# Kernel optimization log

Hardware: AMD Instinct MI355X
Metric: run time of the kernel (lower is better)

The kernel has to match this reference:

```python
import jax, jax.numpy as jnp
import numpy as np

B, N, D, H, P = 8, 1025, 768, 12, 32  # n = P*P + 1 (CLS + patches)
HD = D // H
EPS = 1e-5


def setup_inputs() -> dict:
    key = jax.random.key(0)
    ks = jax.random.split(key, 6)
    return {
        "x": jax.random.normal(ks[0], (B, N, D), dtype=jnp.float32),
        "canny": jax.random.uniform(ks[1], (B, 1, P, P), dtype=jnp.float32),
        "noise": jax.random.uniform(ks[2], (B, P, P), dtype=jnp.float32),
        "ln_w": jnp.ones((D,), dtype=jnp.float32),
        "ln_b": jnp.zeros((D,), dtype=jnp.float32),
        "w_qkv": (jax.random.normal(ks[3], (D, 3 * D), dtype=jnp.float32) * 0.02),
        "w_out": (jax.random.normal(ks[4], (D, D), dtype=jnp.float32) * 0.02),
        "b_out": jnp.zeros((D,), dtype=jnp.float32),
    }


def reference(x, canny, noise, ln_w, ln_b, w_qkv, w_out, b_out):
    b, n, d = x.shape
    # LayerNorm
    mu = jnp.mean(x, axis=-1, keepdims=True)
    var = jnp.mean(jnp.square(x - mu), axis=-1, keepdims=True)
    x_norm = (x - mu) * jax.lax.rsqrt(var + EPS) * ln_w + ln_b
    # QKV projection (no bias), split into heads: [b, n, 3, h, hd]
    qkv = (x_norm @ w_qkv).reshape(b, n, 3, H, HD)
    q = jnp.transpose(qkv[:, :, 0], (0, 2, 1, 3))  # [b, h, n, hd]
    k = jnp.transpose(qkv[:, :, 1], (0, 2, 1, 3))
    v = jnp.transpose(qkv[:, :, 2], (0, 2, 1, 3))
    # NOTE: source uses scale = dim ** -0.5 (full dim, not head_dim)
    dots = jnp.einsum('bhid,bhjd->bhij', q, k) * (d ** -0.5)
    # CLS-row prior injection: softmax over patch keys of CLS query row
    attn_row = jax.nn.softmax(dots[:, :, 0, 1:], axis=-1)  # [b, h, n-1]
    canny_flat = canny.reshape(b, -1) + 1.0                # [b, n-1]
    canny_flat = canny_flat / jnp.sum(canny_flat, axis=-1, keepdims=True)
    noise_flat = noise.reshape(b, -1)                      # [b, n-1]
    noise_flat = noise_flat / jnp.sum(noise_flat, axis=-1, keepdims=True)
    attn_row = attn_row + canny_flat[:, None, :] + noise_flat[:, None, :]
    dots = dots.at[:, :, 0, 1:].set(attn_row)
    # Second (full) softmax; dropout is identity in eval mode
    attn = jax.nn.softmax(dots, axis=-1)
    out = jnp.einsum('bhij,bhjd->bhid', attn, v)           # [b, h, n, hd]
    out = jnp.transpose(out, (0, 2, 1, 3)).reshape(b, n, d)
    return out @ w_out + b_out
```

## Files before the change

### kernel.cpp

```cpp
#include <hip/hip_runtime.h>

#define B_ 8
#define N_ 1025
#define D_ 768
#define H_ 12
#define NP_ 1024
#define ROWS_ (B_*N_)
#define ROWS_PAD_ 8320
#define QKVC_ 2304
#define SCALE_ 0.03608439182435161f
#define EPS_ 1e-5f

typedef float f32x4 __attribute__((ext_vector_type(4)));
typedef short s16x8 __attribute__((ext_vector_type(8)));

#define GLD16(g, l) __builtin_amdgcn_global_load_lds( \
    (const __attribute__((address_space(1))) unsigned int*)(g), \
    (__attribute__((address_space(3))) unsigned int*)(l), 16, 0, 0)

__device__ __forceinline__ float blo(unsigned int u){
  union { unsigned int i; float f; } v; v.i = u << 16; return v.f;
}
__device__ __forceinline__ float bhi(unsigned int u){
  union { unsigned int i; float f; } v; v.i = u & 0xffff0000u; return v.f;
}
__device__ __forceinline__ float bf2f(unsigned short u){
  union { unsigned int i; float f; } v; v.i = ((unsigned int)u) << 16; return v.f;
}
__device__ __forceinline__ unsigned short f2bf(float f){
  union { unsigned int i; float f; } v; v.f = f;
  unsigned int b = v.i;
  b = b + 0x7fffu + ((b >> 16) & 1u);
  return (unsigned short)(b >> 16);
}
__device__ __forceinline__ unsigned int pkbf2(float a, float b){
  union { float f; unsigned int i; } ua, ub;
  ua.f = a; ub.f = b;
  return __builtin_amdgcn_perm(ub.i + 0x8000u, ua.i + 0x8000u, 0x07060302u);
}

__global__ __launch_bounds__(256) void transpose_f2b2(
    const float* __restrict__ w1, unsigned short* __restrict__ d1,
    const float* __restrict__ w2, unsigned short* __restrict__ d2) {
  __shared__ unsigned short tile[32][33];
  int bx = blockIdx.x;
  const float* src; unsigned short* dst; int N, nb;
  if (bx < 72) { src = w1; dst = d1; N = QKVC_; nb = bx * 32; }
  else         { src = w2; dst = d2; N = D_;    nb = (bx - 72) * 32; }
  int kb = blockIdx.y * 32;
  int tx = threadIdx.x & 31, ty = threadIdx.x >> 5;
  #pragma unroll
  for (int i = 0; i < 4; i++) {
    int r = ty + i * 8;
    tile[r][tx] = f2bf(src[(size_t)(kb + r) * N + nb + tx]);
  }
  __syncthreads();
  #pragma unroll
  for (int i = 0; i < 4; i++) {
    int r = ty + i * 8;
    dst[(size_t)(nb + r) * D_ + kb + tx] = tile[tx][r];
  }
}

__global__ __launch_bounds__(256) void layernorm_k(
    const float* __restrict__ x, const float* __restrict__ w,
    const float* __restrict__ b, unsigned short* __restrict__ xn) {
  int row = blockIdx.x;
  int t = threadIdx.x;
  const float* xr = x + (size_t)row * D_;
  float v0 = xr[t], v1 = xr[t + 256], v2 = xr[t + 512];
  float s = v0 + v1 + v2;
  float q = v0 * v0 + v1 * v1 + v2 * v2;
  #pragma unroll
  for (int off = 32; off > 0; off >>= 1) {
    s += __shfl_xor(s, off, 64);
    q += __shfl_xor(q, off, 64);
  }
  __shared__ float r8[8];
  int wv = t >> 6;
  if ((t & 63) == 0) { r8[wv] = s; r8[4 + wv] = q; }
  __syncthreads();
  s = r8[0] + r8[1] + r8[2] + r8[3];
  q = r8[4] + r8[5] + r8[6] + r8[7];
  float mean = s * (1.0f / 768.0f);
  float var = q * (1.0f / 768.0f) - mean * mean;
  var = var < 0.f ? 0.f : var;
  float rstd = rsqrtf(var + EPS_);
  unsigned short* yr = xn + (size_t)row * D_;
  yr[t]       = f2bf((v0 - mean) * rstd * w[t]       + b[t]);
  yr[t + 256] = f2bf((v1 - mean) * rstd * w[t + 256] + b[t + 256]);
  yr[t + 512] = f2bf((v2 - mean) * rstd * w[t + 512] + b[t + 512]);
}

template <bool OF32>
__global__ __launch_bounds__(256) void gemm_bt(
    const unsigned short* __restrict__ A, const unsigned short* __restrict__ Bt,
    void* __restrict__ Cv, const float* __restrict__ bias,
    int Mvalid, int Nn, int Kk) {
  __shared__ short sh[16384];
  short (*As)[4096] = (short (*)[4096])sh;
  short (*Bs)[4096] = (short (*)[4096])(sh + 8192);
  int t = threadIdx.x;
  int bm = blockIdx.y * 128, bn = blockIdx.x * 128;
  int lane = t & 63, wave = t >> 6;
  int wm = (wave & 1) * 64, wn = (wave >> 1) * 64;
  int m16 = lane & 15, quad = lane >> 4;
  f32x4 acc[4][4];
  #pragma unroll
  for (int i = 0; i < 4; i++)
    #pragma unroll
    for (int j = 0; j < 4; j++) acc[i][j] = (f32x4){0.f, 0.f, 0.f, 0.f};

  int e0 = t * 8;
  int e1 = (t + 256) * 8;
  int r0 = e0 >> 5, c0 = e0 & 31;
  int r1 = e1 >> 5, c1 = e1 & 31;
  const unsigned short* a0p = A + (size_t)(bm + r0) * Kk + c0;
  const unsigned short* a1p = A + (size_t)(bm + r1) * Kk + c1;
  const unsigned short* b0p = Bt + (size_t)(bn + r0) * Kk + c0;
  const unsigned short* b1p = Bt + (size_t)(bn + r1) * Kk + c1;

  int ksteps = Kk >> 6;
  for (int kt = 0; kt < ksteps; kt++) {
    int k0 = kt * 64, k1 = kt * 64 + 32;
    __syncthreads();
    GLD16(a0p + k0, &As[0][e0]);
    GLD16(a1p + k0, &As[0][e1]);
    GLD16(a0p + k1, &As[1][e0]);
    GLD16(a1p + k1, &As[1][e1]);
    GLD16(b0p + k0, &Bs[0][e0]);
    GLD16(b1p + k0, &Bs[0][e1]);
    GLD16(b0p + k1, &Bs[1][e0]);
    GLD16(b1p + k1, &Bs[1][e1]);
    __syncthreads();
    #pragma unroll
    for (int hh = 0; hh < 2; hh++) {
      s16x8 af[4], bfr[4];
      #pragma unroll
      for (int i = 0; i < 4; i++) {
        af[i]  = *(const s16x8*)(&As[hh][(wm + i * 16 + m16) * 32 + quad * 8]);
        bfr[i] = *(const s16x8*)(&Bs[hh][(wn + i * 16 + m16) * 32 + quad * 8]);
      }
      #pragma unroll
      for (int i = 0; i < 4; i++)
        #pragma unroll
        for (int j = 0; j < 4; j++)
          acc[i][j] = __builtin_amdgcn_mfma_f32_16x16x32_bf16(af[i], bfr[j], acc[i][j], 0, 0, 0);
    }
  }
  if (!OF32) {
    unsigned short* C = (unsigned short*)Cv;
    __syncthreads();
    #pragma unroll
    for (int j = 0; j < 4; j++) {
      int col = wn + j * 16 + m16;
      #pragma unroll
      for (int i = 0; i < 4; i++)
        #pragma unroll
        for (int r = 0; r < 4; r++)
          sh[(wm + i * 16 + quad * 4 + r) * 128 + col] = (short)f2bf(acc[i][j][r]);
    }
    __syncthreads();
    #pragma unroll
    for (int c = 0; c < 8; c++) {
      int idx = c * 256 + t;
      int row = idx >> 4, col = (idx & 15) * 8;
      if (bm + row < Mvalid)
        *(uint4*)(&C[(size_t)(bm + row) * Nn + bn + col]) = *(const uint4*)(&sh[row * 128 + col]);
    }
  } else {
    float* Cf = (float*)Cv;
    float* shf = (float*)sh;
    #pragma unroll
    for (int half = 0; half < 2; half++) {
      __syncthreads();
      if ((wn >> 6) == half) {
        #pragma unroll
        for (int j = 0; j < 4; j++) {
          int col_l = wn + j * 16 + m16;
          float bv = bias ? bias[bn + col_l] : 0.f;
          #pragma unroll
          for (int i = 0; i < 4; i++)
            #pragma unroll
            for (int r = 0; r < 4; r++)
              shf[(wm + i * 16 + quad * 4 + r) * 64 + (col_l & 63)] = acc[i][j][r] + bv;
        }
      }
      __syncthreads();
      #pragma unroll
      for (int c = 0; c < 8; c++) {
        int idx = c * 256 + t;
        int row = idx >> 4, col = (idx & 15) * 4;
        if (bm + row < Mvalid)
          *(float4*)(&Cf[(size_t)(bm + row) * Nn + bn + half * 64 + col]) =
              *(const float4*)(&shf[row * 64 + col]);
      }
    }
  }
}

__device__ __forceinline__ float block_sum(float v, float* red) {
  int t = threadIdx.x;
  red[t] = v;
  __syncthreads();
  for (int st = 128; st > 0; st >>= 1) {
    if (t < st) red[t] += red[t + st];
    __syncthreads();
  }
  float r = red[0];
  __syncthreads();
  return r;
}

__global__ __launch_bounds__(256) void attn_cls(
    const unsigned short* __restrict__ qkv, const float* __restrict__ canny,
    const float* __restrict__ noise, unsigned short* __restrict__ attn_out) {
  int bh = blockIdx.x;
  int b = bh / H_, h = bh % H_;
  int t = threadIdx.x;
  __shared__ float s[N_];
  __shared__ float red[256];
  __shared__ float q[64];
  __shared__ float pvred[64 * 33];

  if (t < 64) q[t] = bf2f(qkv[(size_t)(b * N_) * QKVC_ + h * 64 + t]);
  __syncthreads();

  for (int j = t; j < N_; j += 256) {
    const unsigned short* krow = qkv + (size_t)(b * N_ + j) * QKVC_ + D_ + h * 64;
    float dot = 0.f;
    #pragma unroll
    for (int c = 0; c < 8; c++) {
      uint4 kk = *(const uint4*)(krow + c * 8);
      dot += q[c*8+0]*blo(kk.x) + q[c*8+1]*bhi(kk.x)
           + q[c*8+2]*blo(kk.y) + q[c*8+3]*bhi(kk.y)
           + q[c*8+4]*blo(kk.z) + q[c*8+5]*bhi(kk.z)
           + q[c*8+6]*blo(kk.w) + q[c*8+7]*bhi(kk.w);
    }
    s[j] = dot * SCALE_;
  }
  float cp = 0.f, npp = 0.f;
  for (int j = t; j < NP_; j += 256) {
    cp  += canny[b * NP_ + j] + 1.0f;
    npp += noise[b * NP_ + j];
  }
  float csum = block_sum(cp, red);
  float nsum = block_sum(npp, red);
  float e1 = 0.f;
  for (int j = t; j < N_; j += 256) if (j >= 1) e1 += __expf(s[j]);
  float sum1 = block_sum(e1, red);
  for (int j = t; j < N_; j += 256) {
    if (j >= 1) {
      s[j] = __expf(s[j]) / sum1
           + (canny[b * NP_ + j - 1] + 1.0f) / csum
           + noise[b * NP_ + j - 1] / nsum;
    }
  }
  __syncthreads();
  float e2 = 0.f;
  for (int j = t; j < N_; j += 256) { float e = __expf(s[j]); s[j] = e; e2 += e; }
  float sum2 = block_sum(e2, red);
  {
    int o = t & 7, g = t >> 3;
    float a[8] = {0.f, 0.f, 0.f, 0.f, 0.f, 0.f, 0.f, 0.f};
    for (int j = g; j < N_; j += 32) {
      float sv = s[j];
      uint4 vv = *(const uint4*)(qkv + (size_t)(b * N_ + j) * QKVC_ + 2 * D_ + h * 64 + o * 8);
      a[0] += sv * blo(vv.x); a[1] += sv * bhi(vv.x);
      a[2] += sv * blo(vv.y); a[3] += sv * bhi(vv.y);
      a[4] += sv * blo(vv.z); a[5] += sv * bhi(vv.z);
      a[6] += sv * blo(vv.w); a[7] += sv * bhi(vv.w);
    }
    #pragma unroll
    for (int i = 0; i < 8; i++) pvred[(o * 8 + i) * 33 + g] = a[i];
  }
  __syncthreads();
  if (t < 64) {
    float acc = 0.f;
    #pragma unroll
    for (int u = 0; u < 32; u++) acc += pvred[t * 33 + u];
    attn_out[(size_t)(b * N_) * D_ + h * 64 + t] = f2bf(acc / sum2);
  }
}

__global__ __launch_bounds__(256) void attn_main(
    const unsigned short* __restrict__ qkv, unsigned short* __restrict__ attn_out) {
  int id = blockIdx.x;
  int tile = id / 96;
  int rem = id % 96;
  int h = rem >> 3;
  int b = rem & 7;
  int t = threadIdx.x;
  int lane = t & 63, w = t >> 6;
  int m16 = lane & 15, quad = lane >> 4;

  __shared__ short ps[128 * 72];
  __shared__ short ks[64 * 72];
  __shared__ unsigned int vs[64 * 36];
  __shared__ float tailbuf[256];

  int qbase = 1 + tile * 128;

  {
    int r = t >> 1, seg = (t & 1) * 32;
    const uint4* src = (const uint4*)(qkv + (size_t)(b * N_ + qbase + r) * QKVC_ + h * 64 + seg);
    uint4 u0 = src[0], u1 = src[1], u2 = src[2], u3 = src[3];
    *(uint4*)(&ps[r * 72 + seg])      = u0;
    *(uint4*)(&ps[r * 72 + seg + 8])  = u1;
    *(uint4*)(&ps[r * 72 + seg + 16]) = u2;
    *(uint4*)(&ps[r * 72 + seg + 24]) = u3;
  }
  s16x8 qb[2][2];
  #pragma unroll
  for (int nt = 0; nt < 2; nt++)
    #pragma unroll
    for (int ks_ = 0; ks_ < 2; ks_++) {
      qb[nt][ks_] = *(const s16x8*)(&ps[(w * 32 + nt * 16 + m16) * 72 + ks_ * 32 + quad * 8]);
      unsigned int* u = (unsigned int*)&qb[nt][ks_];
      #pragma unroll
      for (int i = 0; i < 4; i++)
        u[i] = pkbf2(blo(u[i]) * SCALE_, bhi(u[i]) * SCALE_);
    }
  s16x8 vone;
  #pragma unroll
  for (int i = 0; i < 8; i++) vone[i] = (short)0x3F80;

  f32x4 oacc[2][4], lacc[2];
  #pragma unroll
  for (int mt = 0; mt < 2; mt++) {
    lacc[mt] = (f32x4){0.f, 0.f, 0.f, 0.f};
    #pragma unroll
    for (int dt = 0; dt < 4; dt++) oacc[mt][dt] = (f32x4){0.f, 0.f, 0.f, 0.f};
  }

  int kkey = t >> 2, kseg = (t & 3) * 16;
  const unsigned short* kbase = qkv + (size_t)(b * N_) * QKVC_ + D_ + h * 64;
  int vp2 = t & 31, vseg = t >> 5;
  const unsigned short* vbase = qkv + (size_t)(b * N_) * QKVC_ + 2 * D_ + h * 64 + vseg * 8;
  uint4 kr0, kr1, vr0, vr1;
  {
    const uint4* ksrc = (const uint4*)(kbase + (size_t)kkey * QKVC_ + kseg);
    kr0 = ksrc[0]; kr1 = ksrc[1];
    vr0 = *(const uint4*)(vbase + (size_t)(2 * vp2) * QKVC_);
    vr1 = *(const uint4*)(vbase + (size_t)(2 * vp2 + 1) * QKVC_);
  }

  for (int jt = 0; jt < 16; jt++) {
    __syncthreads();
    *(uint4*)(&ks[kkey * 72 + kseg])     = kr0;
    *(uint4*)(&ks[kkey * 72 + kseg + 8]) = kr1;
    {
      const unsigned int* vaw = (const unsigned int*)&vr0;
      const unsigned int* vbw = (const unsigned int*)&vr1;
      #pragma unroll
      for (int i = 0; i < 4; i++) {
        vs[(vseg * 8 + 2 * i)     * 36 + vp2] = __builtin_amdgcn_perm(vbw[i], vaw[i], 0x05040100u);
        vs[(vseg * 8 + 2 * i + 1) * 36 + vp2] = __builtin_amdgcn_perm(vbw[i], vaw[i], 0x07060302u);
      }
    }
    __syncthreads();
    if (jt < 15) {
      int j0 = (jt + 1) * 64;
      const uint4* ksrc = (const uint4*)(kbase + (size_t)(j0 + kkey) * QKVC_ + kseg);
      kr0 = ksrc[0]; kr1 = ksrc[1];
      vr0 = *(const uint4*)(vbase + (size_t)(j0 + 2 * vp2) * QKVC_);
      vr1 = *(const uint4*)(vbase + (size_t)(j0 + 2 * vp2 + 1) * QKVC_);
    }
    f32x4 sacc[4][2];
    #pragma unroll
    for (int kt = 0; kt < 4; kt++) {
      s16x8 ka0 = *(const s16x8*)(&ks[(kt * 16 + m16) * 72 + quad * 8]);
      s16x8 ka1 = *(const s16x8*)(&ks[(kt * 16 + m16) * 72 + 32 + quad * 8]);
      #pragma unroll
      for (int nt = 0; nt < 2; nt++) {
        f32x4 s = (f32x4){0.f, 0.f, 0.f, 0.f};
        s = __builtin_amdgcn_mfma_f32_16x16x32_bf16(ka0, qb[nt][0], s, 0, 0, 0);
        s = __builtin_amdgcn_mfma_f32_16x16x32_bf16(ka1, qb[nt][1], s, 0, 0, 0);
        sacc[kt][nt] = s;
      }
    }
    #pragma unroll
    for (int kt = 0; kt < 4; kt++) {
      #pragma unroll
      for (int nt = 0; nt < 2; nt++) {
        f32x4 s = sacc[kt][nt];
        float p0 = __expf(s[0]);
        float p1 = __expf(s[1]);
        float p2 = __expf(s[2]);
        float p3 = __expf(s[3]);
        uint2 pk = {pkbf2(p0, p1), pkbf2(p2, p3)};
        *(uint2*)(&ps[(w * 32 + nt * 16 + m16) * 72 + kt * 16 + quad * 4]) = pk;
      }
    }
    __syncthreads();
    s16x8 pa[2][2];
    #pragma unroll
    for (int mt = 0; mt < 2; mt++)
      #pragma unroll
      for (int ks_ = 0; ks_ < 2; ks_++)
        pa[mt][ks_] = *(const s16x8*)(&ps[(w * 32 + mt * 16 + m16) * 72 + ks_ * 32 + quad * 8]);
    const short* vss = (const short*)vs;
    #pragma unroll
    for (int dt = 0; dt < 4; dt++) {
      s16x8 vb0 = *(const s16x8*)(&vss[(dt * 16 + m16) * 72 + quad * 8]);
      s16x8 vb1 = *(const s16x8*)(&vss[(dt * 16 + m16) * 72 + 32 + quad * 8]);
      #pragma unroll
      for (int mt = 0; mt < 2; mt++) {
        oacc[mt][dt] = __builtin_amdgcn_mfma_f32_16x16x32_bf16(pa[mt][0], vb0, oacc[mt][dt], 0, 0, 0);
        oacc[mt][dt] = __builtin_amdgcn_mfma_f32_16x16x32_bf16(pa[mt][1], vb1, oacc[mt][dt], 0, 0, 0);
      }
    }
    #pragma unroll
    for (int mt = 0; mt < 2; mt++) {
      lacc[mt] = __builtin_amdgcn_mfma_f32_16x16x32_bf16(pa[mt][0], vone, lacc[mt], 0, 0, 0);
      lacc[mt] = __builtin_amdgcn_mfma_f32_16x16x32_bf16(pa[mt][1], vone, lacc[mt], 0, 0, 0);
    }
  }
  if (t < 64)       tailbuf[t]             = bf2f(qkv[(size_t)(b * N_ + 1024) * QKVC_ + D_     + h * 64 + t]);
  else if (t < 128) tailbuf[64 + (t - 64)] = bf2f(qkv[(size_t)(b * N_ + 1024) * QKVC_ + 2 * D_ + h * 64 + (t - 64)]);
  __syncthreads();
  #pragma unroll
  for (int nt = 0; nt < 2; nt++) {
    float d = 0.f;
    #pragma unroll
    for (int jj = 0; jj < 8; jj++) {
      d += bf2f((unsigned short)qb[nt][0][jj]) * tailbuf[quad * 8 + jj];
      d += bf2f((unsigned short)qb[nt][1][jj]) * tailbuf[32 + quad * 8 + jj];
    }
    d += __shfl_xor(d, 16, 64);
    d += __shfl_xor(d, 32, 64);
    float p = __expf(d);
    if (quad == 0) tailbuf[128 + w * 32 + nt * 16 + m16] = p;
  }
  __syncthreads();
  #pragma unroll
  for (int mt = 0; mt < 2; mt++)
    #pragma unroll
    for (int r = 0; r < 4; r++) {
      float pr = tailbuf[128 + w * 32 + mt * 16 + quad * 4 + r];
      lacc[mt][r] += pr;
      #pragma unroll
      for (int dt = 0; dt < 4; dt++)
        oacc[mt][dt][r] += pr * tailbuf[64 + dt * 16 + m16];
    }
  #pragma unroll
  for (int mt = 0; mt < 2; mt++) {
    float rinv[4];
    #pragma unroll
    for (int r = 0; r < 4; r++) rinv[r] = 1.0f / lacc[mt][r];
    #pragma unroll
    for (int dt = 0; dt < 4; dt++) {
      #pragma unroll
      for (int r = 0; r < 4; r++) {
        int grow = b * N_ + qbase + w * 32 + mt * 16 + quad * 4 + r;
        attn_out[(size_t)grow * D_ + h * 64 + dt * 16 + m16] = f2bf(oacc[mt][dt][r] * rinv[r]);
      }
    }
  }
}

extern "C" void kernel_launch(void* const* d_in, const int* in_sizes, int n_in,
                              void* d_out, int out_size, void* d_ws, size_t ws_size,
                              hipStream_t stream) {
  (void)in_sizes; (void)n_in; (void)out_size; (void)ws_size;
  const float* x     = (const float*)d_in[0];
  const float* canny = (const float*)d_in[1];
  const float* noise = (const float*)d_in[2];
  const float* lnw   = (const float*)d_in[3];
  const float* lnb   = (const float*)d_in[4];
  const float* wqkv  = (const float*)d_in[5];
  const float* wout  = (const float*)d_in[6];
  const float* bout  = (const float*)d_in[7];
  float* out = (float*)d_out;
  char* ws = (char*)d_ws;

  unsigned short* xn    = (unsigned short*)(ws);
  unsigned short* wqkvT = (unsigned short*)(ws + 12779520);
  unsigned short* woutT = (unsigned short*)(ws + 16318464);
  unsigned short* qkv   = (unsigned short*)(ws + 17498112);

  transpose_f2b2<<<dim3(96, 24), 256, 0, stream>>>(wqkv, wqkvT, wout, woutT);
  layernorm_k<<<dim3(ROWS_), 256, 0, stream>>>(x, lnw, lnb, xn);
  gemm_bt<false><<<dim3(QKVC_ / 128, ROWS_PAD_ / 128), 256, 0, stream>>>(
      xn, wqkvT, (void*)qkv, nullptr, ROWS_, QKVC_, D_);
  attn_cls<<<dim3(B_ * H_), 256, 0, stream>>>(qkv, canny, noise, xn);
  attn_main<<<dim3(8 * H_ * B_), 256, 0, stream>>>(qkv, xn);
  gemm_bt<true><<<dim3(D_ / 128, ROWS_PAD_ / 128), 256, 0, stream>>>(
      xn, woutT, (void*)out, bout, ROWS_, D_, D_);
}
```

Before: 222.2 us.

## Rewrite bf16 GEMM with 128x256 tiles, double-buffered LDS prefetch, XCD-aware block mapping

The bf16 GEMM used for the QKV and output projections now uses 512-thread blocks computing 128x256 tiles. It double-buffers the A and B tiles in LDS, issuing global-to-LDS loads two k-steps ahead and waiting with a partial vmcnt before each barrier. LDS addresses are XOR-swizzled to avoid bank conflicts, MFMA sections raise wave priority, and a 1D grid is remapped so neighbouring tiles land on the same XCD for L2 reuse. The aim is to hide global load latency and improve MFMA utilisation, at the cost of more LDS (96 KB) and fewer blocks, with 2304/768 columns needing to divide by 256.

```diff
diff --git a/kernel.cpp b/kernel.cpp
--- a/kernel.cpp
+++ b/kernel.cpp
@@ -93,80 +93,153 @@
 }
 
 template <bool OF32>
-__global__ __launch_bounds__(256) void gemm_bt(
+__global__ __launch_bounds__(512) void gemm_bt(
     const unsigned short* __restrict__ A, const unsigned short* __restrict__ Bt,
     void* __restrict__ Cv, const float* __restrict__ bias,
     int Mvalid, int Nn, int Kk) {
-  __shared__ short sh[16384];
-  short (*As)[4096] = (short (*)[4096])sh;
-  short (*Bs)[4096] = (short (*)[4096])(sh + 8192);
+  __shared__ short sh[49152];
+  short* shA = sh;
+  short* shB = sh + 16384;
+
   int t = threadIdx.x;
-  int bm = blockIdx.y * 128, bn = blockIdx.x * 128;
-  int lane = t & 63, wave = t >> 6;
-  int wm = (wave & 1) * 64, wn = (wave >> 1) * 64;
+  int lane = t & 63, w = t >> 6;
   int m16 = lane & 15, quad = lane >> 4;
+
+  int nwg = gridDim.x;
+  int nbx = Nn >> 8;
+  int id = blockIdx.x;
+  int qq = nwg >> 3, rr = nwg & 7;
+  int xcd = id & 7, off = id >> 3;
+  int wg = (xcd < rr ? xcd * (qq + 1) : rr * (qq + 1) + (xcd - rr) * qq) + off;
+  int bx = wg % nbx, by = wg / nbx;
+  int bm = by * 128, bn = bx * 256;
+
+  int wm = (w >> 2) * 64, wn = (w & 3) * 64;
+
   f32x4 acc[4][4];
   #pragma unroll
   for (int i = 0; i < 4; i++)
     #pragma unroll
     for (int j = 0; j < 4; j++) acc[i][j] = (f32x4){0.f, 0.f, 0.f, 0.f};
 
-  int e0 = t * 8;
-  int e1 = (t + 256) * 8;
-  int r0 = e0 >> 5, c0 = e0 & 31;
-  int r1 = e1 >> 5, c1 = e1 & 31;
-  const unsigned short* a0p = A + (size_t)(bm + r0) * Kk + c0;
-  const unsigned short* a1p = A + (size_t)(bm + r1) * Kk + c1;
-  const unsigned short* b0p = Bt + (size_t)(bn + r0) * Kk + c0;
-  const unsigned short* b1p = Bt + (size_t)(bn + r1) * Kk + c1;
-
-  int ksteps = Kk >> 6;
-  for (int kt = 0; kt < ksteps; kt++) {
-    int k0 = kt * 64, k1 = kt * 64 + 32;
-    __syncthreads();
-    GLD16(a0p + k0, &As[0][e0]);
-    GLD16(a1p + k0, &As[0][e1]);
-    GLD16(a0p + k1, &As[1][e0]);
-    GLD16(a1p + k1, &As[1][e1]);
-    GLD16(b0p + k0, &Bs[0][e0]);
-    GLD16(b1p + k0, &Bs[0][e1]);
-    GLD16(b0p + k1, &Bs[1][e0]);
-    GLD16(b1p + k1, &Bs[1][e1]);
-    __syncthreads();
-    #pragma unroll
-    for (int hh = 0; hh < 2; hh++) {
-      s16x8 af[4], bfr[4];
-      #pragma unroll
-      for (int i = 0; i < 4; i++) {
-        af[i]  = *(const s16x8*)(&As[hh][(wm + i * 16 + m16) * 32 + quad * 8]);
-        bfr[i] = *(const s16x8*)(&Bs[hh][(wn + i * 16 + m16) * 32 + quad * 8]);
-      }
-      #pragma unroll
-      for (int i = 0; i < 4; i++)
-        #pragma unroll
-        for (int j = 0; j < 4; j++)
-          acc[i][j] = __builtin_amdgcn_mfma_f32_16x16x32_bf16(af[i], bfr[j], acc[i][j], 0, 0, 0);
-    }
-  }
+  int lrs = t >> 3, slot8 = t & 7;
+  const unsigned short* aA = A + (size_t)(bm + (lrs >> 5) * 64 + (lrs & 31)) * Kk
+                               + ((slot8 ^ (lrs & 7)) * 8);
+  int lcs = t >> 2, slot4 = t & 3;
+  const unsigned short* bB0 = Bt + (size_t)(bn + lcs) * Kk + ((slot4 ^ (lcs & 3)) * 8);
+  const unsigned short* bB1 = bB0 + (size_t)128 * Kk;
+
+  int lrA = (w >> 2) * 32 + m16;
+  int sA0 = ((0 + quad) ^ (m16 & 7)) * 8;
+  int sA1 = ((4 + quad) ^ (m16 & 7)) * 8;
+  int lcB = wn + m16;
+  int sB  = (quad ^ (m16 & 3)) * 8;
+
+  int KS = Kk >> 6;
+
+#define STAGE_A(BUF, MH, KT) GLD16(aA + (size_t)(MH) * 32 * Kk + (KT) * 64, \
+                                   shA + ((BUF) * 2 + (MH)) * 4096 + t * 8)
+#define STAGE_B(BUF, KSL, KT) do { \
+    GLD16(bB0 + (KT) * 64 + (KSL) * 32, shB + ((BUF) * 2 + (KSL)) * 8192 + t * 8); \
+    GLD16(bB1 + (KT) * 64 + (KSL) * 32, shB + ((BUF) * 2 + (KSL)) * 8192 + t * 8 + 4096); \
+  } while (0)
+#define VMB6() do { asm volatile("s_waitcnt vmcnt(6)" ::: "memory"); \
+                    __builtin_amdgcn_s_barrier(); } while (0)
+
+  {
+    int kp = KS > 1 ? 1 : 0;
+    STAGE_A(0, 0, 0);
+    STAGE_B(0, 0, 0);
+    STAGE_B(0, 1, 0);
+    STAGE_A(0, 1, 0);
+    STAGE_A(1, 0, kp);
+    STAGE_B(1, 0, kp);
+    STAGE_B(1, 1, kp);
+    VMB6();
+  }
+
+#define KTILE(BUF, KTV) do { \
+    int kn1 = (KTV) + 1 < KS ? (KTV) + 1 : KS - 1; \
+    int kn2 = (KTV) + 2 < KS ? (KTV) + 2 : KS - 1; \
+    s16x8 bfr[4][2]; \
+     \
+    STAGE_A((BUF) ^ 1, 1, kn1); \
+    { \
+      const short* sa = shA + ((BUF) * 2 + 0) * 4096; \
+      s16x8 a0k0 = *(const s16x8*)(sa + lrA * 64 + sA0); \
+      s16x8 a0k1 = *(const s16x8*)(sa + lrA * 64 + sA1); \
+      s16x8 a1k0 = *(const s16x8*)(sa + (lrA + 16) * 64 + sA0); \
+      s16x8 a1k1 = *(const s16x8*)(sa + (lrA + 16) * 64 + sA1); \
+      const short* sb0 = shB + ((BUF) * 2 + 0) * 8192; \
+      const short* sb1 = shB + ((BUF) * 2 + 1) * 8192; \
+      _Pragma("unroll") \
+      for (int b = 0; b < 4; b++) { \
+        bfr[b][0] = *(const s16x8*)(sb0 + (lcB + b * 16) * 32 + sB); \
+        bfr[b][1] = *(const s16x8*)(sb1 + (lcB + b * 16) * 32 + sB); \
+      } \
+      __builtin_amdgcn_s_setprio(1); \
+      _Pragma("unroll") \
+      for (int b = 0; b < 4; b++) { \
+        acc[0][b] = __builtin_amdgcn_mfma_f32_16x16x32_bf16(a0k0, bfr[b][0], acc[0][b], 0, 0, 0); \
+        acc[0][b] = __builtin_amdgcn_mfma_f32_16x16x32_bf16(a0k1, bfr[b][1], acc[0][b], 0, 0, 0); \
+        acc[1][b] = __builtin_amdgcn_mfma_f32_16x16x32_bf16(a1k0, bfr[b][0], acc[1][b], 0, 0, 0); \
+        acc[1][b] = __builtin_amdgcn_mfma_f32_16x16x32_bf16(a1k1, bfr[b][1], acc[1][b], 0, 0, 0); \
+      } \
+      __builtin_amdgcn_s_setprio(0); \
+    } \
+    VMB6(); \
+     \
+    STAGE_A(BUF, 0, kn2); \
+    STAGE_B(BUF, 0, kn2); \
+    STAGE_B(BUF, 1, kn2); \
+    { \
+      const short* sa = shA + ((BUF) * 2 + 1) * 4096; \
+      s16x8 a0k0 = *(const s16x8*)(sa + lrA * 64 + sA0); \
+      s16x8 a0k1 = *(const s16x8*)(sa + lrA * 64 + sA1); \
+      s16x8 a1k0 = *(const s16x8*)(sa + (lrA + 16) * 64 + sA0); \
+      s16x8 a1k1 = *(const s16x8*)(sa + (lrA + 16) * 64 + sA1); \
+      __builtin_amdgcn_s_setprio(1); \
+      _Pragma("unroll") \
+      for (int b = 0; b < 4; b++) { \
+        acc[2][b] = __builtin_amdgcn_mfma_f32_16x16x32_bf16(a0k0, bfr[b][0], acc[2][b], 0, 0, 0); \
+        acc[2][b] = __builtin_amdgcn_mfma_f32_16x16x32_bf16(a0k1, bfr[b][1], acc[2][b], 0, 0, 0); \
+        acc[3][b] = __builtin_amdgcn_mfma_f32_16x16x32_bf16(a1k0, bfr[b][0], acc[3][b], 0, 0, 0); \
+        acc[3][b] = __builtin_amdgcn_mfma_f32_16x16x32_bf16(a1k1, bfr[b][1], acc[3][b], 0, 0, 0); \
+      } \
+      __builtin_amdgcn_s_setprio(0); \
+    } \
+    VMB6(); \
+  } while (0)
+
+  int nk2 = KS >> 1;
+  for (int k2 = 0; k2 < nk2; k2++) {
+    KTILE(0, k2 * 2);
+    KTILE(1, k2 * 2 + 1);
+  }
+  asm volatile("s_waitcnt vmcnt(0)" ::: "memory");
+  __builtin_amdgcn_s_barrier();
+
+#undef KTILE
+#undef STAGE_A
+#undef STAGE_B
+#undef VMB6
+
   if (!OF32) {
     unsigned short* C = (unsigned short*)Cv;
-    __syncthreads();
-    #pragma unroll
-    for (int j = 0; j < 4; j++) {
-      int col = wn + j * 16 + m16;
-      #pragma unroll
-      for (int i = 0; i < 4; i++)
+    #pragma unroll
+    for (int a = 0; a < 4; a++)
+      #pragma unroll
+      for (int b = 0; b < 4; b++)
         #pragma unroll
         for (int r = 0; r < 4; r++)
-          sh[(wm + i * 16 + quad * 4 + r) * 128 + col] = (short)f2bf(acc[i][j][r]);
-    }
+          sh[(wm + a * 16 + quad * 4 + r) * 256 + wn + b * 16 + m16] = (short)f2bf(acc[a][b][r]);
     __syncthreads();
     #pragma unroll
     for (int c = 0; c < 8; c++) {
-      int idx = c * 256 + t;
-      int row = idx >> 4, col = (idx & 15) * 8;
+      int idx = c * 512 + t;
+      int row = idx >> 5, col = (idx & 31) * 8;
       if (bm + row < Mvalid)
-        *(uint4*)(&C[(size_t)(bm + row) * Nn + bn + col]) = *(const uint4*)(&sh[row * 128 + col]);
+        *(uint4*)(&C[(size_t)(bm + row) * Nn + bn + col]) = *(const uint4*)(&sh[row * 256 + col]);
     }
   } else {
     float* Cf = (float*)Cv;
@@ -174,26 +247,27 @@
     #pragma unroll
     for (int half = 0; half < 2; half++) {
       __syncthreads();
-      if ((wn >> 6) == half) {
+      if ((wn >> 7) == half) {
         #pragma unroll
-        for (int j = 0; j < 4; j++) {
-          int col_l = wn + j * 16 + m16;
-          float bv = bias ? bias[bn + col_l] : 0.f;
+        for (int b = 0; b < 4; b++) {
+          int colg = bn + wn + b * 16 + m16;
+          float bv = bias ? bias[colg] : 0.f;
+          int coll = (wn & 127) + b * 16 + m16;
           #pragma unroll
-          for (int i = 0; i < 4; i++)
+          for (int a = 0; a < 4; a++)
             #pragma unroll
             for (int r = 0; r < 4; r++)
-              shf[(wm + i * 16 + quad * 4 + r) * 64 + (col_l & 63)] = acc[i][j][r] + bv;
+              shf[(wm + a * 16 + quad * 4 + r) * 128 + coll] = acc[a][b][r] + bv;
         }
       }
       __syncthreads();
       #pragma unroll
       for (int c = 0; c < 8; c++) {
-        int idx = c * 256 + t;
-        int row = idx >> 4, col = (idx & 15) * 4;
+        int idx = c * 512 + t;
+        int row = idx >> 5, col = (idx & 31) * 4;
         if (bm + row < Mvalid)
-          *(float4*)(&Cf[(size_t)(bm + row) * Nn + bn + half * 64 + col]) =
-              *(const float4*)(&shf[row * 64 + col]);
+          *(float4*)(&Cf[(size_t)(bm + row) * Nn + bn + half * 128 + col]) =
+              *(const float4*)(&shf[row * 128 + col]);
       }
     }
   }
@@ -481,10 +555,10 @@
 
   transpose_f2b2<<<dim3(96, 24), 256, 0, stream>>>(wqkv, wqkvT, wout, woutT);
   layernorm_k<<<dim3(ROWS_), 256, 0, stream>>>(x, lnw, lnb, xn);
-  gemm_bt<false><<<dim3(QKVC_ / 128, ROWS_PAD_ / 128), 256, 0, stream>>>(
+  gemm_bt<false><<<dim3((QKVC_ / 256) * (ROWS_PAD_ / 128)), 512, 0, stream>>>(
       xn, wqkvT, (void*)qkv, nullptr, ROWS_, QKVC_, D_);
   attn_cls<<<dim3(B_ * H_), 256, 0, stream>>>(qkv, canny, noise, xn);
   attn_main<<<dim3(8 * H_ * B_), 256, 0, stream>>>(qkv, xn);
-  gemm_bt<true><<<dim3(D_ / 128, ROWS_PAD_ / 128), 256, 0, stream>>>(
+  gemm_bt<true><<<dim3((D_ / 256) * (ROWS_PAD_ / 128)), 512, 0, stream>>>(
       xn, woutT, (void*)out, bout, ROWS_, D_, D_);
 }
```

Measured after the change: 223.4 us. No clear change (+0.5%).

## Double-buffer GEMM LDS tiles with XOR swizzle and XCD-aware block remap

Applied to the files above, without the earlier changes.

The bf16 GEMM is rewritten to prefetch the next 64-wide K slice into a second LDS buffer while MFMAs consume the current one. The tile layout is XOR-swizzled to avoid LDS bank conflicts, and s_setprio is raised around the MFMA bursts. The grid is flattened and remapped so consecutive tiles land on the same XCD for L2 reuse. The fp32 epilogue writes the full 128-column tile in one pass. This doubles LDS use to 64KB per block, which may lower occupancy.

```diff
diff --git a/kernel.cpp b/kernel.cpp
--- a/kernel.cpp
+++ b/kernel.cpp
@@ -97,60 +97,81 @@
     const unsigned short* __restrict__ A, const unsigned short* __restrict__ Bt,
     void* __restrict__ Cv, const float* __restrict__ bias,
     int Mvalid, int Nn, int Kk) {
-  __shared__ short sh[16384];
-  short (*As)[4096] = (short (*)[4096])sh;
-  short (*Bs)[4096] = (short (*)[4096])(sh + 8192);
+  __shared__ short sh[32768];
   int t = threadIdx.x;
-  int bm = blockIdx.y * 128, bn = blockIdx.x * 128;
-  int lane = t & 63, wave = t >> 6;
-  int wm = (wave & 1) * 64, wn = (wave >> 1) * 64;
+  int lane = t & 63, w = t >> 6;
   int m16 = lane & 15, quad = lane >> 4;
+
+  int nwg = gridDim.x;
+  int nbx = Nn >> 7;
+  int id = blockIdx.x;
+  int qq = nwg >> 3, rr = nwg & 7;
+  int xcd = id & 7, off = id >> 3;
+  int wg = (xcd < rr ? xcd * (qq + 1) : rr * (qq + 1) + (xcd - rr) * qq) + off;
+  int bx = wg % nbx, by = wg / nbx;
+  int bm = by * 128, bn = bx * 128;
+
+  int wm = (w & 1) * 64, wn = (w >> 1) * 64;
+
   f32x4 acc[4][4];
   #pragma unroll
   for (int i = 0; i < 4; i++)
     #pragma unroll
     for (int j = 0; j < 4; j++) acc[i][j] = (f32x4){0.f, 0.f, 0.f, 0.f};
 
-  int e0 = t * 8;
-  int e1 = (t + 256) * 8;
-  int r0 = e0 >> 5, c0 = e0 & 31;
-  int r1 = e1 >> 5, c1 = e1 & 31;
-  const unsigned short* a0p = A + (size_t)(bm + r0) * Kk + c0;
-  const unsigned short* a1p = A + (size_t)(bm + r1) * Kk + c1;
-  const unsigned short* b0p = Bt + (size_t)(bn + r0) * Kk + c0;
-  const unsigned short* b1p = Bt + (size_t)(bn + r1) * Kk + c1;
-
-  int ksteps = Kk >> 6;
-  for (int kt = 0; kt < ksteps; kt++) {
-    int k0 = kt * 64, k1 = kt * 64 + 32;
-    __syncthreads();
-    GLD16(a0p + k0, &As[0][e0]);
-    GLD16(a1p + k0, &As[0][e1]);
-    GLD16(a0p + k1, &As[1][e0]);
-    GLD16(a1p + k1, &As[1][e1]);
-    GLD16(b0p + k0, &Bs[0][e0]);
-    GLD16(b1p + k0, &Bs[0][e1]);
-    GLD16(b0p + k1, &Bs[1][e0]);
-    GLD16(b1p + k1, &Bs[1][e1]);
-    __syncthreads();
-    #pragma unroll
-    for (int hh = 0; hh < 2; hh++) {
+  const unsigned short* aP[4];
+  const unsigned short* bP[4];
+  #pragma unroll
+  for (int c = 0; c < 4; c++) {
+    int g = t + c * 256;
+    int row = g >> 3, slot = g & 7;
+    aP[c] = A  + (size_t)(bm + row) * Kk + ((slot ^ (row & 7)) * 8);
+    bP[c] = Bt + (size_t)(bn + row) * Kk + ((slot ^ (row & 7)) * 8);
+  }
+
+  int KS = Kk >> 6;
+  int cur = 0;
+  #pragma unroll
+  for (int c = 0; c < 4; c++) GLD16(aP[c], sh + (t + c * 256) * 8);
+  #pragma unroll
+  for (int c = 0; c < 4; c++) GLD16(bP[c], sh + 16384 + (t + c * 256) * 8);
+
+  for (int kt = 0; kt < KS; kt++) {
+    asm volatile("s_waitcnt vmcnt(0)" ::: "memory");
+    __builtin_amdgcn_s_barrier();
+    if (kt + 1 < KS) {
+      int nb2 = (cur ^ 1) * 8192;
+      int ko = (kt + 1) * 64;
+      #pragma unroll
+      for (int c = 0; c < 4; c++) GLD16(aP[c] + ko, sh + nb2 + (t + c * 256) * 8);
+      #pragma unroll
+      for (int c = 0; c < 4; c++) GLD16(bP[c] + ko, sh + 16384 + nb2 + (t + c * 256) * 8);
+    }
+    const short* sa = sh + cur * 8192;
+    const short* sb = sh + 16384 + cur * 8192;
+    #pragma unroll
+    for (int ks = 0; ks < 2; ks++) {
+      int so = ((ks * 4 + quad) ^ (m16 & 7)) * 8;
       s16x8 af[4], bfr[4];
       #pragma unroll
       for (int i = 0; i < 4; i++) {
-        af[i]  = *(const s16x8*)(&As[hh][(wm + i * 16 + m16) * 32 + quad * 8]);
-        bfr[i] = *(const s16x8*)(&Bs[hh][(wn + i * 16 + m16) * 32 + quad * 8]);
+        af[i]  = *(const s16x8*)(sa + (wm + i * 16 + m16) * 64 + so);
+        bfr[i] = *(const s16x8*)(sb + (wn + i * 16 + m16) * 64 + so);
       }
+      __builtin_amdgcn_s_setprio(1);
       #pragma unroll
       for (int i = 0; i < 4; i++)
         #pragma unroll
         for (int j = 0; j < 4; j++)
           acc[i][j] = __builtin_amdgcn_mfma_f32_16x16x32_bf16(af[i], bfr[j], acc[i][j], 0, 0, 0);
-    }
-  }
+      __builtin_amdgcn_s_setprio(0);
+    }
+    cur ^= 1;
+  }
+  __syncthreads();
+
   if (!OF32) {
     unsigned short* C = (unsigned short*)Cv;
-    __syncthreads();
     #pragma unroll
     for (int j = 0; j < 4; j++) {
       int col = wn + j * 16 + m16;
@@ -172,29 +193,23 @@
     float* Cf = (float*)Cv;
     float* shf = (float*)sh;
     #pragma unroll
-    for (int half = 0; half < 2; half++) {
-      __syncthreads();
-      if ((wn >> 6) == half) {
+    for (int j = 0; j < 4; j++) {
+      int col = wn + j * 16 + m16;
+      float bv = bias ? bias[bn + col] : 0.f;
+      #pragma unroll
+      for (int i = 0; i < 4; i++)
         #pragma unroll
-        for (int j = 0; j < 4; j++) {
-          int col_l = wn + j * 16 + m16;
-          float bv = bias ? bias[bn + col_l] : 0.f;
-          #pragma unroll
-          for (int i = 0; i < 4; i++)
-            #pragma unroll
-            for (int r = 0; r < 4; r++)
-              shf[(wm + i * 16 + quad * 4 + r) * 64 + (col_l & 63)] = acc[i][j][r] + bv;
-        }
-      }
-      __syncthreads();
-      #pragma unroll
-      for (int c = 0; c < 8; c++) {
-        int idx = c * 256 + t;
-        int row = idx >> 4, col = (idx & 15) * 4;
-        if (bm + row < Mvalid)
-          *(float4*)(&Cf[(size_t)(bm + row) * Nn + bn + half * 64 + col]) =
-              *(const float4*)(&shf[row * 64 + col]);
-      }
+        for (int r = 0; r < 4; r++)
+          shf[(wm + i * 16 + quad * 4 + r) * 128 + col] = acc[i][j][r] + bv;
+    }
+    __syncthreads();
+    #pragma unroll
+    for (int c = 0; c < 16; c++) {
+      int idx = c * 256 + t;
+      int row = idx >> 5, col = (idx & 31) * 4;
+      if (bm + row < Mvalid)
+        *(float4*)(&Cf[(size_t)(bm + row) * Nn + bn + col]) =
+            *(const float4*)(&shf[row * 128 + col]);
     }
   }
 }
@@ -481,10 +496,10 @@
 
   transpose_f2b2<<<dim3(96, 24), 256, 0, stream>>>(wqkv, wqkvT, wout, woutT);
   layernorm_k<<<dim3(ROWS_), 256, 0, stream>>>(x, lnw, lnb, xn);
-  gemm_bt<false><<<dim3(QKVC_ / 128, ROWS_PAD_ / 128), 256, 0, stream>>>(
+  gemm_bt<false><<<dim3((QKVC_ / 128) * (ROWS_PAD_ / 128)), 256, 0, stream>>>(
       xn, wqkvT, (void*)qkv, nullptr, ROWS_, QKVC_, D_);
   attn_cls<<<dim3(B_ * H_), 256, 0, stream>>>(qkv, canny, noise, xn);
   attn_main<<<dim3(8 * H_ * B_), 256, 0, stream>>>(qkv, xn);
-  gemm_bt<true><<<dim3(D_ / 128, ROWS_PAD_ / 128), 256, 0, stream>>>(
+  gemm_bt<true><<<dim3((D_ / 128) * (ROWS_PAD_ / 128)), 256, 0, stream>>>(
       xn, woutT, (void*)out, bout, ROWS_, D_, D_);
 }
```

After: 217.4 us. 1.02x faster.
